# Kernel tuning notes

Measured on AMD Instinct MI355X. Metric: run time of the kernel, lower is better.

Reference implementation:

```python
import jax, jax.numpy as jnp
import numpy as np

N, F, B, H = 4096, 64, 16, 8  # nodes, feat dim, graphs, GAT heads


def _graph():
    # symmetric random graph (avg deg ~8), plus exact 2-hop and 3-hop edge lists
    # (this reproduces torch_sparse.spspmm with coalesced=True on the boolean structure)
    rng = np.random.default_rng(0)
    s = rng.integers(0, N, 8192)
    d = rng.integers(0, N, 8192)
    m = s != d
    s, d = s[m], d[m]
    rows = np.concatenate([s, d]).astype(np.int64)
    cols = np.concatenate([d, s]).astype(np.int64)
    key = np.unique(rows * N + cols)
    rows, cols = key // N, key % N
    A = np.zeros((N, N), np.float32)
    A[rows, cols] = 1.0
    A2 = (A @ A) > 0
    A3 = (A2.astype(np.float32) @ A) > 0
    np.fill_diagonal(A2, False)  # GATConv/GCNConv remove then re-add self-loops
    np.fill_diagonal(A3, False)
    e1 = np.stack([rows, cols]).astype(np.int64)
    e2 = np.stack(np.nonzero(A2)).astype(np.int64)
    e3 = np.stack(np.nonzero(A3)).astype(np.int64)
    return e1, e2, e3


def _sl(ei, n):
    loops = jnp.arange(n, dtype=ei.dtype)
    return jnp.concatenate([ei, jnp.stack([loops, loops])], axis=1)


def _seg_softmax(logits, seg, n):
    m = jax.ops.segment_max(logits, seg, num_segments=n)
    e = jnp.exp(logits - m[seg])
    s = jax.ops.segment_sum(e, seg, num_segments=n)
    return e / s[seg]


def _gat(x, ei, W, a_src, a_dst, b, heads):
    # PyG GATConv: per-head linear, edge attention logits, softmax over incoming edges
    n = x.shape[0]
    d = a_src.shape[1]
    h = (x @ W).reshape(n, heads, d)  # [N,H,D]
    src, dst = ei[0], ei[1]
    al = jnp.einsum('nhd,hd->nh', h, a_src)
    ar = jnp.einsum('nhd,hd->nh', h, a_dst)
    logit = jax.nn.leaky_relu(al[src] + ar[dst], 0.2)  # [E,H]
    alpha = _seg_softmax(logit, dst, n)
    out = jax.ops.segment_sum(alpha[:, :, None] * h[src], dst, num_segments=n)
    return out.reshape(n, heads * d) + b


def _gcn(x, ei, W, b):
    n = x.shape[0]
    src, dst = ei[0], ei[1]
    h = x @ W
    deg = jax.ops.segment_sum(jnp.ones(src.shape, x.dtype), dst, num_segments=n)
    dinv = jnp.where(deg > 0, deg ** -0.5, 0.0)
    norm = dinv[src] * dinv[dst]
    return jax.ops.segment_sum(norm[:, None] * h[src], dst, num_segments=n) + b


def setup_inputs():
    key = jax.random.key(0)
    ks = iter(jax.random.split(key, 40))
    e1, e2, e3 = _graph()
    p = lambda *shape: jax.random.normal(next(ks), shape, jnp.float32) * 0.1
    return dict(
        x=jax.random.normal(next(ks), (N, F), jnp.float32),
        edge_index=jnp.asarray(e1), edge_index2=jnp.asarray(e2), edge_index3=jnp.asarray(e3),
        batch=jnp.asarray(np.repeat(np.arange(B), N // B)),
        g1_W=p(F, H * F), g1_as=p(H, F), g1_ad=p(H, F), g1_b=p(H * F),
        g2_W=p(H * F, F), g2_as=p(1, F), g2_ad=p(1, F), g2_b=p(F),
        gfc_W=p(F, F), gfc_b=p(F), gfc1_W=p(F, 128), gfc1_b=p(128),
        gout_W=p(128, F), gout_b=p(F),
        c2_W=p(F, 2 * F), c2_b=p(2 * F), c3_W=p(2 * F, 4 * F), c3_b=p(4 * F),
        A_W=p(4 * F, F), A_b=p(F), B_W=p(2 * F, F), B_b=p(F),
        Wih=p(F, 3 * F), Whh=p(F, 3 * F), bih=p(3 * F), bhh=p(3 * F),
        f1_W=p(F, 128), f1_b=p(128), f2_W=p(128, 120), f2_b=p(120),
    )


def reference(x, edge_index, edge_index2, edge_index3, batch,
              g1_W, g1_as, g1_ad, g1_b, g2_W, g2_as, g2_ad, g2_b,
              gfc_W, gfc_b, gfc1_W, gfc1_b, gout_W, gout_b,
              c2_W, c2_b, c3_W, c3_b, A_W, A_b, B_W, B_b,
              Wih, Whh, bih, bhh, f1_W, f1_b, f2_W, f2_b):
    n = x.shape[0]
    e1, e2, e3 = _sl(edge_index, n), _sl(edge_index2, n), _sl(edge_index3, n)

    def gat_block(xin, ei):  # inner GAT module (eval mode: dropouts are identity)
        h = jax.nn.elu(_gat(xin, ei, g1_W, g1_as, g1_ad, g1_b, H))
        h = jax.nn.relu(_gat(h, ei, g2_W, g2_as, g2_ad, g2_b, 1))
        h = jax.nn.relu(h @ gfc_W + gfc_b)
        h = jax.nn.relu(h @ gfc1_W + gfc1_b)
        return h @ gout_W + gout_b

    h1 = jax.nn.relu(gat_block(x, e1))
    h2 = jax.nn.relu(_gcn(h1, e1, c2_W, c2_b))
    h3 = jax.nn.relu(_gcn(h2, e1, c3_W, c3_b))            # [N,4F]
    h4 = jax.nn.relu(gat_block(x, e2))
    h5 = jax.nn.relu(_gcn(h4, e2, c2_W, c2_b))            # [N,2F]
    h6 = jax.nn.relu(gat_block(x, e3))                     # [N,F]

    # GateUpdate
    b_ = h5 @ B_W + B_b
    a_ = h3 @ A_W + A_b
    z = jax.nn.sigmoid(a_ + b_)
    hg = z * b_ + (1 - z) * a_
    # GRUCell(h6, hg)
    gi = h6 @ Wih + bih
    gh = hg @ Whh + bhh
    r = jax.nn.sigmoid(gi[:, :F] + gh[:, :F])
    zz = jax.nn.sigmoid(gi[:, F:2 * F] + gh[:, F:2 * F])
    nn_ = jnp.tanh(gi[:, 2 * F:] + r * gh[:, 2 * F:])
    cc = (1 - zz) * nn_ + zz * hg

    g = jax.ops.segment_max(cc, batch, num_segments=B)    # global_max_pool -> [B,F]
    g = jax.nn.relu(g @ f1_W + f1_b)
    return g @ f2_W + f2_b                                 # [B,120]
```

## Files before the change

### kernel.cpp

```cpp
#include <hip/hip_runtime.h>
#include <math.h>

#define NN 4096
#define NG 16
#define WB() __builtin_amdgcn_wave_barrier()

__global__ void rowptr3_kernel(const int* __restrict__ ea, int Ea,
                               const int* __restrict__ eb, int Eb,
                               const int* __restrict__ ec, int Ec,
                               int* __restrict__ rpa, int* __restrict__ rpb, int* __restrict__ rpc){
    int t = blockIdx.x * blockDim.x + threadIdx.x;
    int set = t / (NN + 1), i = t % (NN + 1);
    if (set >= 3) return;
    const int* e0 = set == 0 ? ea : set == 1 ? eb : ec;
    int E        = set == 0 ? Ea : set == 1 ? Eb : Ec;
    int* rp      = set == 0 ? rpa : set == 1 ? rpb : rpc;
    if (i == NN){ rp[NN] = E; return; }
    int lo = 0, hi = E;
    while (lo < hi){ int mid = (lo + hi) >> 1; if (e0[mid] < i) lo = mid + 1; else hi = mid; }
    rp[i] = lo;
}

__global__ void dinv2_kernel(const int* __restrict__ rp1, const int* __restrict__ rp2,
                             float* __restrict__ dinv1, float* __restrict__ dinv2){
    int t = blockIdx.x * blockDim.x + threadIdx.x;
    int set = t >> 12, i = t & (NN - 1);
    if (set >= 2) return;
    const int* rp = set ? rp2 : rp1;
    float deg = (float)(rp[i+1] - rp[i] + 1);
    (set ? dinv2 : dinv1)[i] = 1.0f / sqrtf(deg);
}

__global__ __launch_bounds__(256)
void gemm_kernel(const float* __restrict__ A, const float* __restrict__ W,
                 const float* __restrict__ bias, float* __restrict__ C,
                 int K, int Nc, int act){
    __shared__ float As[64][17];
    __shared__ float Bs[16][64];
    const int tid = threadIdx.x;
    const int tx = tid & 15, ty = tid >> 4;
    const int row0 = blockIdx.y * 64, col0 = blockIdx.x * 64;
    float acc[4][4] = {};
    for (int k0 = 0; k0 < K; k0 += 16){
        {   int idx = tid * 4; int r = idx >> 4, kk = idx & 15;
            float4 av = *reinterpret_cast<const float4*>(&A[(size_t)(row0 + r) * K + k0 + kk]);
            As[r][kk+0]=av.x; As[r][kk+1]=av.y; As[r][kk+2]=av.z; As[r][kk+3]=av.w; }
        {   int idx = tid * 4; int r = idx >> 6, cc = idx & 63;
            float4 wv = *reinterpret_cast<const float4*>(&W[(size_t)(k0 + r) * Nc + col0 + cc]);
            *reinterpret_cast<float4*>(&Bs[r][cc]) = wv; }
        __syncthreads();
        #pragma unroll
        for (int kk = 0; kk < 16; ++kk){
            float a[4], b[4];
            #pragma unroll
            for (int i = 0; i < 4; ++i) a[i] = As[ty*4+i][kk];
            #pragma unroll
            for (int j = 0; j < 4; ++j) b[j] = Bs[kk][tx*4+j];
            #pragma unroll
            for (int i = 0; i < 4; ++i)
                #pragma unroll
                for (int j = 0; j < 4; ++j) acc[i][j] += a[i]*b[j];
        }
        __syncthreads();
    }
    #pragma unroll
    for (int i = 0; i < 4; ++i){
        int r = row0 + ty*4 + i;
        #pragma unroll
        for (int j = 0; j < 4; ++j){
            int c = col0 + tx*4 + j;
            float v = acc[i][j] + (bias ? bias[c] : 0.0f);
            if (act == 1) v = fmaxf(v, 0.0f);
            C[(size_t)r * Nc + c] = v;
        }
    }
}

__global__ __launch_bounds__(256)
void gemm32_kernel(const float* __restrict__ A, const float* __restrict__ W,
                   const float* __restrict__ bias, float* __restrict__ C,
                   int K, int Nc, int act){
    __shared__ float As[32][17];
    __shared__ float Bs[16][64];
    const int tid = threadIdx.x;
    const int tx = tid & 15, ty = tid >> 4;
    const int row0 = blockIdx.y * 32, col0 = blockIdx.x * 64;
    float acc[2][4] = {};
    for (int k0 = 0; k0 < K; k0 += 16){
        {   int idx = tid * 2; int r = idx >> 4, kk = idx & 15;
            float2 av = *reinterpret_cast<const float2*>(&A[(size_t)(row0 + r) * K + k0 + kk]);
            As[r][kk] = av.x; As[r][kk+1] = av.y; }
        {   int idx = tid * 4; int r = idx >> 6, cc = idx & 63;
            *reinterpret_cast<float4*>(&Bs[r][cc]) =
                *reinterpret_cast<const float4*>(&W[(size_t)(k0 + r) * Nc + col0 + cc]); }
        __syncthreads();
        #pragma unroll
        for (int kk = 0; kk < 16; ++kk){
            float a0 = As[ty*2][kk], a1 = As[ty*2+1][kk];
            float b[4];
            #pragma unroll
            for (int j = 0; j < 4; ++j) b[j] = Bs[kk][tx*4+j];
            #pragma unroll
            for (int j = 0; j < 4; ++j){ acc[0][j] += a0*b[j]; acc[1][j] += a1*b[j]; }
        }
        __syncthreads();
    }
    #pragma unroll
    for (int i = 0; i < 2; ++i){
        int r = row0 + ty*2 + i;
        #pragma unroll
        for (int j = 0; j < 4; ++j){
            int c = col0 + tx*4 + j;
            float v = acc[i][j] + (bias ? bias[c] : 0.0f);
            if (act == 1) v = fmaxf(v, 0.0f);
            C[(size_t)r * Nc + c] = v;
        }
    }
}

__global__ __launch_bounds__(256)
void attn_dot8_kernel(const float* __restrict__ h,
                      const float* __restrict__ a_src, const float* __restrict__ a_dst,
                      float* __restrict__ al, float* __restrict__ ar){
    const int lane = threadIdx.x & 63, wid = threadIdx.x >> 6;
    const int n = blockIdx.x * 4 + wid;
    float x[8], y[8];
    #pragma unroll
    for (int c = 0; c < 8; ++c){
        float v = h[(size_t)n*512 + c*64 + lane];
        x[c] = v * a_src[c*64 + lane];
        y[c] = v * a_dst[c*64 + lane];
    }
    #pragma unroll
    for (int off = 1; off < 64; off <<= 1){
        #pragma unroll
        for (int c = 0; c < 8; ++c){
            x[c] += __shfl_xor(x[c], off);
            y[c] += __shfl_xor(y[c], off);
        }
    }
    if (lane == 0){
        #pragma unroll
        for (int c = 0; c < 8; ++c){ al[n*8 + c] = x[c]; ar[n*8 + c] = y[c]; }
    }
}

__global__ __launch_bounds__(256)
void attn_dot1_kernel(const float* __restrict__ h,
                      const float* __restrict__ a_src, const float* __restrict__ a_dst,
                      float* __restrict__ al, float* __restrict__ ar){
    const int lane = threadIdx.x & 63, wid = threadIdx.x >> 6;
    const int n = blockIdx.x * 4 + wid;
    float v = h[(size_t)n*64 + lane];
    float x = v * a_src[lane], y = v * a_dst[lane];
    #pragma unroll
    for (int off = 1; off < 64; off <<= 1){ x += __shfl_xor(x, off); y += __shfl_xor(y, off); }
    if (lane == 0){ al[n] = x; ar[n] = y; }
}

__global__ __launch_bounds__(64)
void gat_agg8_wave_kernel(const float* __restrict__ hfeat,
                          const float* __restrict__ al, const float* __restrict__ ar,
                          const int* __restrict__ rpA, const int* __restrict__ rpB, const int* __restrict__ rpC,
                          const int* __restrict__ clA, const int* __restrict__ clB, const int* __restrict__ clC,
                          const float* __restrict__ bias, float* __restrict__ out){
    const int bid = blockIdx.x;
    const int set = bid >> 12, i = bid & (NN - 1);
    const int lane = threadIdx.x;
    const int* rowptr = set == 0 ? rpA : set == 1 ? rpB : rpC;
    const int* cols   = set == 0 ? clA : set == 1 ? clB : clC;
    const int start = rowptr[i], end = rowptr[i+1];
    const int deg = end - start;

    float al_i[8], ar_i[8];
    {
        float4 t0 = *reinterpret_cast<const float4*>(&al[(size_t)i*8]);
        float4 t1 = *reinterpret_cast<const float4*>(&al[(size_t)i*8+4]);
        al_i[0]=t0.x; al_i[1]=t0.y; al_i[2]=t0.z; al_i[3]=t0.w;
        al_i[4]=t1.x; al_i[5]=t1.y; al_i[6]=t1.z; al_i[7]=t1.w;
        float4 u0 = *reinterpret_cast<const float4*>(&ar[(size_t)i*8]);
        float4 u1 = *reinterpret_cast<const float4*>(&ar[(size_t)i*8+4]);
        ar_i[0]=u0.x; ar_i[1]=u0.y; ar_i[2]=u0.z; ar_i[3]=u0.w;
        ar_i[4]=u1.x; ar_i[5]=u1.y; ar_i[6]=u1.z; ar_i[7]=u1.w;
    }

    float m[8], s[8];
    #pragma unroll
    for (int h = 0; h < 8; ++h){ m[h] = -1e30f; s[h] = 0.f; }
    for (int k = start + lane; k < end; k += 64){
        int j = cols[k];
        float4 t0 = *reinterpret_cast<const float4*>(&al[(size_t)j*8]);
        float4 t1 = *reinterpret_cast<const float4*>(&al[(size_t)j*8+4]);
        float av[8] = {t0.x,t0.y,t0.z,t0.w,t1.x,t1.y,t1.z,t1.w};
        #pragma unroll
        for (int h = 0; h < 8; ++h){
            float x = av[h] + ar_i[h];
            x = x >= 0.f ? x : 0.2f * x;
            float mn = fmaxf(m[h], x);
            s[h] = s[h] * __expf(m[h] - mn) + __expf(x - mn);
            m[h] = mn;
        }
    }
    if (lane == 0){
        #pragma unroll
        for (int h = 0; h < 8; ++h){
            float x = al_i[h] + ar_i[h];
            x = x >= 0.f ? x : 0.2f * x;
            float mn = fmaxf(m[h], x);
            s[h] = s[h] * __expf(m[h] - mn) + __expf(x - mn);
            m[h] = mn;
        }
    }
    #pragma unroll
    for (int off = 1; off < 64; off <<= 1){
        #pragma unroll
        for (int h = 0; h < 8; ++h){
            float m2 = __shfl_xor(m[h], off), s2 = __shfl_xor(s[h], off);
            float mn = fmaxf(m[h], m2);
            s[h] = s[h] * __expf(m[h] - mn) + s2 * __expf(m2 - mn);
            m[h] = mn;
        }
    }

    __shared__ int   sbuf[64];
    __shared__ float wbuf[64][9];
    const int c0 = 4*lane, c1 = 256 + 4*lane;
    const int h0 = lane >> 4, h1 = 4 + h0;
    float4 A0 = {0.f,0.f,0.f,0.f}, A1 = {0.f,0.f,0.f,0.f};
    for (int k0 = 0; k0 < deg; k0 += 64){
        int cnt = min(64, deg - k0);
        if (lane < cnt) sbuf[lane] = cols[start + k0 + lane];
        __syncthreads();
        if (lane < cnt){
            int j = sbuf[lane];
            float4 t0 = *reinterpret_cast<const float4*>(&al[(size_t)j*8]);
            float4 t1 = *reinterpret_cast<const float4*>(&al[(size_t)j*8+4]);
            float av[8] = {t0.x,t0.y,t0.z,t0.w,t1.x,t1.y,t1.z,t1.w};
            #pragma unroll
            for (int h = 0; h < 8; ++h){
                float x = av[h] + ar_i[h];
                x = x >= 0.f ? x : 0.2f * x;
                wbuf[lane][h] = __expf(x - m[h]);
            }
        }
        __syncthreads();
        int e = 0;
        for (; e + 4 <= cnt; e += 4){
            int j0 = sbuf[e], j1 = sbuf[e+1], j2 = sbuf[e+2], j3 = sbuf[e+3];
            const float* q0 = &hfeat[(size_t)j0*512];
            const float* q1 = &hfeat[(size_t)j1*512];
            const float* q2 = &hfeat[(size_t)j2*512];
            const float* q3 = &hfeat[(size_t)j3*512];
            float4 v00 = *reinterpret_cast<const float4*>(q0 + c0);
            float4 v01 = *reinterpret_cast<const float4*>(q0 + c1);
            float4 v10 = *reinterpret_cast<const float4*>(q1 + c0);
            float4 v11 = *reinterpret_cast<const float4*>(q1 + c1);
            float4 v20 = *reinterpret_cast<const float4*>(q2 + c0);
            float4 v21 = *reinterpret_cast<const float4*>(q2 + c1);
            float4 v30 = *reinterpret_cast<const float4*>(q3 + c0);
            float4 v31 = *reinterpret_cast<const float4*>(q3 + c1);
            float w00 = wbuf[e  ][h0], w01 = wbuf[e  ][h1];
            float w10 = wbuf[e+1][h0], w11 = wbuf[e+1][h1];
            float w20 = wbuf[e+2][h0], w21 = wbuf[e+2][h1];
            float w30 = wbuf[e+3][h0], w31 = wbuf[e+3][h1];
            A0.x += w00*v00.x; A0.y += w00*v00.y; A0.z += w00*v00.z; A0.w += w00*v00.w;
            A1.x += w01*v01.x; A1.y += w01*v01.y; A1.z += w01*v01.z; A1.w += w01*v01.w;
            A0.x += w10*v10.x; A0.y += w10*v10.y; A0.z += w10*v10.z; A0.w += w10*v10.w;
            A1.x += w11*v11.x; A1.y += w11*v11.y; A1.z += w11*v11.z; A1.w += w11*v11.w;
            A0.x += w20*v20.x; A0.y += w20*v20.y; A0.z += w20*v20.z; A0.w += w20*v20.w;
            A1.x += w21*v21.x; A1.y += w21*v21.y; A1.z += w21*v21.z; A1.w += w21*v21.w;
            A0.x += w30*v30.x; A0.y += w30*v30.y; A0.z += w30*v30.z; A0.w += w30*v30.w;
            A1.x += w31*v31.x; A1.y += w31*v31.y; A1.z += w31*v31.z; A1.w += w31*v31.w;
        }
        for (; e < cnt; ++e){
            int j = sbuf[e];
            const float* hp = &hfeat[(size_t)j*512];
            float w0 = wbuf[e][h0], w1 = wbuf[e][h1];
            float4 v0 = *reinterpret_cast<const float4*>(hp + c0);
            float4 v1 = *reinterpret_cast<const float4*>(hp + c1);
            A0.x += w0*v0.x; A0.y += w0*v0.y; A0.z += w0*v0.z; A0.w += w0*v0.w;
            A1.x += w1*v1.x; A1.y += w1*v1.y; A1.z += w1*v1.z; A1.w += w1*v1.w;
        }
        __syncthreads();
    }
    {
        float x0 = al_i[h0] + ar_i[h0]; x0 = x0 >= 0.f ? x0 : 0.2f*x0;
        float x1 = al_i[h1] + ar_i[h1]; x1 = x1 >= 0.f ? x1 : 0.2f*x1;
        float w0 = __expf(x0 - m[h0]), w1 = __expf(x1 - m[h1]);
        float4 hv0 = *reinterpret_cast<const float4*>(&hfeat[(size_t)i*512 + c0]);
        float4 hv1 = *reinterpret_cast<const float4*>(&hfeat[(size_t)i*512 + c1]);
        A0.x += w0*hv0.x; A0.y += w0*hv0.y; A0.z += w0*hv0.z; A0.w += w0*hv0.w;
        A1.x += w1*hv1.x; A1.y += w1*hv1.y; A1.z += w1*hv1.z; A1.w += w1*hv1.w;
        float inv0 = 1.f / s[h0], inv1 = 1.f / s[h1];
        float4 b0 = *reinterpret_cast<const float4*>(&bias[c0]);
        float4 b1 = *reinterpret_cast<const float4*>(&bias[c1]);
        float4 o0, o1;
        o0.x = A0.x*inv0 + b0.x; o0.y = A0.y*inv0 + b0.y;
        o0.z = A0.z*inv0 + b0.z; o0.w = A0.w*inv0 + b0.w;
        o1.x = A1.x*inv1 + b1.x; o1.y = A1.y*inv1 + b1.y;
        o1.z = A1.z*inv1 + b1.z; o1.w = A1.w*inv1 + b1.w;
        o0.x = o0.x > 0.f ? o0.x : __expf(o0.x) - 1.f;
        o0.y = o0.y > 0.f ? o0.y : __expf(o0.y) - 1.f;
        o0.z = o0.z > 0.f ? o0.z : __expf(o0.z) - 1.f;
        o0.w = o0.w > 0.f ? o0.w : __expf(o0.w) - 1.f;
        o1.x = o1.x > 0.f ? o1.x : __expf(o1.x) - 1.f;
        o1.y = o1.y > 0.f ? o1.y : __expf(o1.y) - 1.f;
        o1.z = o1.z > 0.f ? o1.z : __expf(o1.z) - 1.f;
        o1.w = o1.w > 0.f ? o1.w : __expf(o1.w) - 1.f;
        *reinterpret_cast<float4*>(&out[(size_t)bid*512 + c0]) = o0;
        *reinterpret_cast<float4*>(&out[(size_t)bid*512 + c1]) = o1;
    }
}

template<int BLOCK, int NHEADS>
__global__ __launch_bounds__(BLOCK)
void gat_agg_kernel(const float* __restrict__ hfeat,
                    const float* __restrict__ al, const float* __restrict__ ar,
                    const int* __restrict__ rpA, const int* __restrict__ rpB, const int* __restrict__ rpC,
                    const int* __restrict__ clA, const int* __restrict__ clB, const int* __restrict__ clC,
                    const float* __restrict__ bias, float* __restrict__ out,
                    int act, int sharedfeat){
    constexpr int TD    = NHEADS * 64;
    constexpr int CHUNK = BLOCK / NHEADS;
    const int bid = blockIdx.x;
    const int set = bid >> 12, i = bid & (NN - 1);
    const int tid = threadIdx.x;
    const int* rowptr = set == 0 ? rpA : set == 1 ? rpB : rpC;
    const int* cols   = set == 0 ? clA : set == 1 ? clB : clC;
    const int base = sharedfeat ? 0 : set * NN;
    const int start = rowptr[i], end = rowptr[i+1];

    float al_i[NHEADS], ar_i[NHEADS];
    #pragma unroll
    for (int h = 0; h < NHEADS; ++h){
        al_i[h] = al[(size_t)(base + i)*NHEADS + h];
        ar_i[h] = ar[(size_t)(base + i)*NHEADS + h];
    }
    float m[NHEADS], s[NHEADS];
    #pragma unroll
    for (int h = 0; h < NHEADS; ++h){ m[h] = -1e30f; s[h] = 0.f; }
    for (int k = start + tid; k < end; k += BLOCK){
        int j = cols[k];
        #pragma unroll
        for (int h = 0; h < NHEADS; ++h){
            float x = al[(size_t)(base + j)*NHEADS + h] + ar_i[h];
            x = x >= 0.f ? x : 0.2f * x;
            float mn = fmaxf(m[h], x);
            s[h] = s[h] * __expf(m[h] - mn) + __expf(x - mn);
            m[h] = mn;
        }
    }
    if (tid == 0){
        #pragma unroll
        for (int h = 0; h < NHEADS; ++h){
            float x = al_i[h] + ar_i[h];
            x = x >= 0.f ? x : 0.2f * x;
            float mn = fmaxf(m[h], x);
            s[h] = s[h] * __expf(m[h] - mn) + __expf(x - mn);
            m[h] = mn;
        }
    }
    #pragma unroll
    for (int off = 1; off < 64; off <<= 1){
        #pragma unroll
        for (int h = 0; h < NHEADS; ++h){
            float m2 = __shfl_xor(m[h], off), s2 = __shfl_xor(s[h], off);
            float mn = fmaxf(m[h], m2);
            s[h] = s[h] * __expf(m[h] - mn) + s2 * __expf(m2 - mn);
            m[h] = mn;
        }
    }

    __shared__ int   sbuf[CHUNK];
    __shared__ float wbuf[CHUNK][NHEADS];
    const int deg = end - start;
    float p0 = 0.f, p1 = 0.f, p2 = 0.f, p3 = 0.f;
    for (int k0 = 0; k0 < deg; k0 += CHUNK){
        int cnt = min(CHUNK, deg - k0);
        if (tid < cnt) sbuf[tid] = cols[start + k0 + tid];
        __syncthreads();
        if (tid < cnt){
            float x = al[(size_t)(base + sbuf[tid])*NHEADS] + ar_i[0];
            x = x >= 0.f ? x : 0.2f * x;
            wbuf[tid][0] = __expf(x - m[0]);
        }
        __syncthreads();
        int e = 0;
        for (; e + 8 <= cnt; e += 8){
            int j0 = sbuf[e],   j1 = sbuf[e+1], j2 = sbuf[e+2], j3 = sbuf[e+3];
            int j4 = sbuf[e+4], j5 = sbuf[e+5], j6 = sbuf[e+6], j7 = sbuf[e+7];
            float v0 = hfeat[(size_t)(base + j0)*TD + tid];
            float v1 = hfeat[(size_t)(base + j1)*TD + tid];
            float v2 = hfeat[(size_t)(base + j2)*TD + tid];
            float v3 = hfeat[(size_t)(base + j3)*TD + tid];
            float v4 = hfeat[(size_t)(base + j4)*TD + tid];
            float v5 = hfeat[(size_t)(base + j5)*TD + tid];
            float v6 = hfeat[(size_t)(base + j6)*TD + tid];
            float v7 = hfeat[(size_t)(base + j7)*TD + tid];
            p0 += wbuf[e  ][0] * v0; p1 += wbuf[e+1][0] * v1;
            p2 += wbuf[e+2][0] * v2; p3 += wbuf[e+3][0] * v3;
            p0 += wbuf[e+4][0] * v4; p1 += wbuf[e+5][0] * v5;
            p2 += wbuf[e+6][0] * v6; p3 += wbuf[e+7][0] * v7;
        }
        for (; e < cnt; ++e)
            p0 += wbuf[e][0] * hfeat[(size_t)(base + sbuf[e])*TD + tid];
        __syncthreads();
    }
    float acc = (p0 + p1) + (p2 + p3);
    float x = al_i[0] + ar_i[0];
    x = x >= 0.f ? x : 0.2f * x;
    acc += __expf(x - m[0]) * hfeat[(size_t)(base + i)*TD + tid];
    float v = acc / s[0] + bias[tid];
    if (act == 1) v = fmaxf(v, 0.f);
    else          v = v > 0.f ? v : __expf(v) - 1.f;
    out[(size_t)bid*TD + tid] = v;
}

template<int DIM>
__global__ __launch_bounds__(DIM)
void gcn_agg_kernel(const float* __restrict__ h,
                    const int* __restrict__ rpA, const int* __restrict__ rpB,
                    const int* __restrict__ clA, const int* __restrict__ clB,
                    const float* __restrict__ dvA, const float* __restrict__ dvB,
                    const float* __restrict__ bias, float* __restrict__ out){
    const int bid = blockIdx.x;
    const int set = bid >> 12, i = bid & (NN - 1);
    const int* rowptr = set ? rpB : rpA;
    const int* cols   = set ? clB : clA;
    const float* dinv = set ? dvB : dvA;
    const int c = threadIdx.x;
    const int start = rowptr[i], end = rowptr[i+1];
    const float di = dinv[i];
    const size_t rbase = (size_t)(set * NN) * DIM;
    float self = di * di * h[(size_t)bid * DIM + c];
    float p0 = 0.f, p1 = 0.f, p2 = 0.f, p3 = 0.f;
    int k = start;
    for (; k + 8 <= end; k += 8){
        int j0 = cols[k],   j1 = cols[k+1], j2 = cols[k+2], j3 = cols[k+3];
        int j4 = cols[k+4], j5 = cols[k+5], j6 = cols[k+6], j7 = cols[k+7];
        float v0 = h[rbase + (size_t)j0 * DIM + c];
        float v1 = h[rbase + (size_t)j1 * DIM + c];
        float v2 = h[rbase + (size_t)j2 * DIM + c];
        float v3 = h[rbase + (size_t)j3 * DIM + c];
        float v4 = h[rbase + (size_t)j4 * DIM + c];
        float v5 = h[rbase + (size_t)j5 * DIM + c];
        float v6 = h[rbase + (size_t)j6 * DIM + c];
        float v7 = h[rbase + (size_t)j7 * DIM + c];
        p0 += dinv[j0] * v0; p1 += dinv[j1] * v1;
        p2 += dinv[j2] * v2; p3 += dinv[j3] * v3;
        p0 += dinv[j4] * v4; p1 += dinv[j5] * v5;
        p2 += dinv[j6] * v6; p3 += dinv[j7] * v7;
    }
    for (; k < end; ++k){
        int j = cols[k];
        p0 += dinv[j] * h[rbase + (size_t)j * DIM + c];
    }
    float acc = self + di * ((p0 + p1) + (p2 + p3));
    out[(size_t)bid * DIM + c] = fmaxf(acc + bias[c], 0.f);
}

__global__ __launch_bounds__(256)
void gate_gru_kernel(const float* __restrict__ h3, const float* __restrict__ h5,
                     const float* __restrict__ h6,
                     const float* __restrict__ A_W, const float* __restrict__ A_b,
                     const float* __restrict__ B_W, const float* __restrict__ B_b,
                     const float* __restrict__ Wih, const float* __restrict__ bih,
                     const float* __restrict__ Whh, const float* __restrict__ bhh,
                     float* __restrict__ cc){
    __shared__ float l3[4][256];
    __shared__ float l5[4][128];
    __shared__ float l6[4][64];
    __shared__ float lhg[4][64];
    const int lane = threadIdx.x & 63, wid = threadIdx.x >> 6;
    const int r = blockIdx.x * 4 + wid;
    for (int c = lane; c < 256; c += 64) l3[wid][c] = h3[(size_t)r*256 + c];
    for (int c = lane; c < 128; c += 64) l5[wid][c] = h5[(size_t)r*128 + c];
    l6[wid][lane] = h6[(size_t)r*64 + lane];
    WB();
    float a = A_b[lane];
    #pragma unroll 8
    for (int k = 0; k < 256; ++k) a += l3[wid][k] * A_W[k*64 + lane];
    float b = B_b[lane];
    #pragma unroll 8
    for (int k = 0; k < 128; ++k) b += l5[wid][k] * B_W[k*64 + lane];
    float z = 1.f / (1.f + expf(-(a + b)));
    float hg = z * b + (1.f - z) * a;
    lhg[wid][lane] = hg;
    WB();
    float gi0 = bih[lane], gi1 = bih[64 + lane], gi2 = bih[128 + lane];
    float gh0 = bhh[lane], gh1 = bhh[64 + lane], gh2 = bhh[128 + lane];
    #pragma unroll 4
    for (int k = 0; k < 64; ++k){
        float v6 = l6[wid][k], vh = lhg[wid][k];
        gi0 += v6 * Wih[k*192 + lane];
        gi1 += v6 * Wih[k*192 + 64 + lane];
        gi2 += v6 * Wih[k*192 + 128 + lane];
        gh0 += vh * Whh[k*192 + lane];
        gh1 += vh * Whh[k*192 + 64 + lane];
        gh2 += vh * Whh[k*192 + 128 + lane];
    }
    float rr = 1.f / (1.f + expf(-(gi0 + gh0)));
    float zz = 1.f / (1.f + expf(-(gi1 + gh1)));
    float nn = tanhf(gi2 + rr * gh2);
    cc[(size_t)r*64 + lane] = (1.f - zz) * nn + zz * hg;
}

__global__ __launch_bounds__(256)
void head_kernel(const float* __restrict__ cc,
                 const float* __restrict__ f1_W, const float* __restrict__ f1_b,
                 const float* __restrict__ f2_W, const float* __restrict__ f2_b,
                 float* __restrict__ out){
    const int b = blockIdx.x, tid = threadIdx.x;
    const int c = tid & 63, grp = tid >> 6;
    __shared__ float red4[4][64];
    __shared__ float gmax[64];
    __shared__ float fgs[128];
    const float* base = cc + (size_t)(b * (NN / NG)) * 64;
    float m = -1e30f;
    #pragma unroll 8
    for (int n = grp; n < NN / NG; n += 4) m = fmaxf(m, base[n * 64 + c]);
    red4[grp][c] = m;
    __syncthreads();
    if (tid < 64)
        gmax[tid] = fmaxf(fmaxf(red4[0][tid], red4[1][tid]),
                          fmaxf(red4[2][tid], red4[3][tid]));
    __syncthreads();
    if (tid < 128){
        float acc = 0.f;
        #pragma unroll
        for (int k = 0; k < 64; ++k) acc += gmax[k] * f1_W[k * 128 + tid];
        fgs[tid] = fmaxf(acc + f1_b[tid], 0.f);
    }
    __syncthreads();
    if (tid < 120){
        float acc = 0.f;
        #pragma unroll
        for (int k = 0; k < 128; ++k) acc += fgs[k] * f2_W[k * 120 + tid];
        out[b * 120 + tid] = acc + f2_b[tid];
    }
}

extern "C" void kernel_launch(void* const* d_in, const int* in_sizes, int n_in,
                              void* d_out, int out_size, void* d_ws, size_t ws_size,
                              hipStream_t stream){
    const float* x  = (const float*)d_in[0];
    const int* e1 = (const int*)d_in[1]; const int E1 = in_sizes[1] / 2;
    const int* e2 = (const int*)d_in[2]; const int E2 = in_sizes[2] / 2;
    const int* e3 = (const int*)d_in[3]; const int E3 = in_sizes[3] / 2;
    const float* g1_W  = (const float*)d_in[5];
    const float* g1_as = (const float*)d_in[6];
    const float* g1_ad = (const float*)d_in[7];
    const float* g1_b  = (const float*)d_in[8];
    const float* g2_W  = (const float*)d_in[9];
    const float* g2_as = (const float*)d_in[10];
    const float* g2_ad = (const float*)d_in[11];
    const float* g2_b  = (const float*)d_in[12];
    const float* gfc_W = (const float*)d_in[13];
    const float* gfc_b = (const float*)d_in[14];
    const float* gfc1_W= (const float*)d_in[15];
    const float* gfc1_b= (const float*)d_in[16];
    const float* gout_W= (const float*)d_in[17];
    const float* gout_b= (const float*)d_in[18];
    const float* c2_W  = (const float*)d_in[19];
    const float* c2_b  = (const float*)d_in[20];
    const float* c3_W  = (const float*)d_in[21];
    const float* c3_b  = (const float*)d_in[22];
    const float* A_W   = (const float*)d_in[23];
    const float* A_b   = (const float*)d_in[24];
    const float* B_W   = (const float*)d_in[25];
    const float* B_b   = (const float*)d_in[26];
    const float* Wih   = (const float*)d_in[27];
    const float* Whh   = (const float*)d_in[28];
    const float* bih   = (const float*)d_in[29];
    const float* bhh   = (const float*)d_in[30];
    const float* f1_W  = (const float*)d_in[31];
    const float* f1_b  = (const float*)d_in[32];
    const float* f2_W  = (const float*)d_in[33];
    const float* f2_b  = (const float*)d_in[34];
    float* out = (float*)d_out;

    int* ip = (int*)d_ws;
    int* rp1 = ip; int* rp2 = ip + 4100; int* rp3 = ip + 8200;
    float* fb = (float*)(ip + 12300);
    size_t o = 0;
    auto alloc = [&](size_t nf){ float* p = fb + o; o += nf; return p; };
    float* dinv1 = alloc(NN);
    float* dinv2 = alloc(NN);
    float* hbuf  = alloc((size_t)NN*512);
    float* al1   = alloc((size_t)NN*8);
    float* ar1   = alloc((size_t)NN*8);
    float* bigA  = alloc((size_t)3*NN*512);
    float* t2    = alloc((size_t)3*NN*64);
    float* al2   = alloc((size_t)3*NN);
    float* ar2   = alloc((size_t)3*NN);
    (void)ws_size; (void)n_in; (void)out_size;

    float* eluo3 = bigA;
    float* g2o   = bigA;
    float* fc1   = bigA + (size_t)786432;
    float* fc2   = bigA + (size_t)1572864;
    float* houts = hbuf;
    float* h1    = houts;
    float* h6    = houts + (size_t)2*NN*64;
    float* gcnx2 = bigA + (size_t)3145728;
    float* h25   = bigA + (size_t)4194304;
    float* h2    = h25;
    float* h5    = h25 + (size_t)NN*128;
    float* gcnx3 = bigA;
    float* h3    = bigA + (size_t)1048576;
    float* ccb   = bigA + (size_t)4456448;
    const int* cols1 = e1 + E1; const int* cols2 = e2 + E2; const int* cols3 = e3 + E3;

    rowptr3_kernel<<<(3*(NN+1)+255)/256, 256, 0, stream>>>(e1, E1, e2, E2, e3, E3, rp1, rp2, rp3);
    dinv2_kernel<<<2*NN/256, 256, 0, stream>>>(rp1, rp2, dinv1, dinv2);

    gemm_kernel<<<dim3(8, 64), 256, 0, stream>>>(x, g1_W, nullptr, hbuf, 64, 512, 0);
    attn_dot8_kernel<<<NN/4, 256, 0, stream>>>(hbuf, g1_as, g1_ad, al1, ar1);
    gat_agg8_wave_kernel<<<3*NN, 64, 0, stream>>>(hbuf, al1, ar1,
        rp1, rp2, rp3, cols1, cols2, cols3, g1_b, eluo3);
    gemm32_kernel<<<dim3(1, 384), 256, 0, stream>>>(eluo3, g2_W, nullptr, t2, 512, 64, 0);
    attn_dot1_kernel<<<3*NN/4, 256, 0, stream>>>(t2, g2_as, g2_ad, al2, ar2);
    gat_agg_kernel<64,1><<<3*NN, 64, 0, stream>>>(t2, al2, ar2,
        rp1, rp2, rp3, cols1, cols2, cols3, g2_b, g2o, 1, 0);
    gemm32_kernel<<<dim3(1, 384), 256, 0, stream>>>(g2o, gfc_W, gfc_b, fc1, 64, 64, 1);
    gemm_kernel<<<dim3(2, 192), 256, 0, stream>>>(fc1, gfc1_W, gfc1_b, fc2, 64, 128, 1);
    gemm32_kernel<<<dim3(1, 384), 256, 0, stream>>>(fc2, gout_W, gout_b, houts, 128, 64, 1);

    gemm_kernel<<<dim3(2, 128), 256, 0, stream>>>(houts, c2_W, nullptr, gcnx2, 64, 128, 0);
    gcn_agg_kernel<128><<<2*NN, 128, 0, stream>>>(gcnx2, rp1, rp2, cols1, cols2,
                                                  dinv1, dinv2, c2_b, h25);
    gemm_kernel<<<dim3(4, 64), 256, 0, stream>>>(h2, c3_W, nullptr, gcnx3, 128, 256, 0);
    gcn_agg_kernel<256><<<NN, 256, 0, stream>>>(gcnx3, rp1, rp1, cols1, cols1,
                                                dinv1, dinv1, c3_b, h3);

    gate_gru_kernel<<<NN/4, 256, 0, stream>>>(h3, h5, h6, A_W, A_b, B_W, B_b,
                                              Wih, bih, Whh, bhh, ccb);

    head_kernel<<<NG, 256, 0, stream>>>(ccb, f1_W, f1_b, f2_W, f2_b, out);
}
```

Measured before the change: 376.6 us.

## Split 8-head GAT aggregation into softmax-stats pass and half-head aggregation pass

The fused 8-head GAT aggregation kernel is split in two. A first kernel computes the per-node, per-head softmax max and sum and writes them to new workspace buffers. A second kernel, launched with twice as many blocks, has each block handle 4 heads (256 columns) of one node. This is meant to expose more parallelism and lower per-block latency on high-degree 2-hop and 3-hop neighbourhoods. In exchange it adds a kernel launch, an extra global round trip for the stats, and redundant reads of column indices and attention logits across the two halves.

New measurement: 371.0 us. No clear change (-1.5%).

```diff
diff --git a/kernel.cpp b/kernel.cpp
--- a/kernel.cpp
+++ b/kernel.cpp
@@ -159,18 +159,16 @@
 }
 
 __global__ __launch_bounds__(64)
-void gat_agg8_wave_kernel(const float* __restrict__ hfeat,
-                          const float* __restrict__ al, const float* __restrict__ ar,
-                          const int* __restrict__ rpA, const int* __restrict__ rpB, const int* __restrict__ rpC,
-                          const int* __restrict__ clA, const int* __restrict__ clB, const int* __restrict__ clC,
-                          const float* __restrict__ bias, float* __restrict__ out){
-    const int bid = blockIdx.x;
-    const int set = bid >> 12, i = bid & (NN - 1);
+void attn_ms8_kernel(const float* __restrict__ al, const float* __restrict__ ar,
+                     const int* __restrict__ rpA, const int* __restrict__ rpB, const int* __restrict__ rpC,
+                     const int* __restrict__ clA, const int* __restrict__ clB, const int* __restrict__ clC,
+                     float* __restrict__ m8, float* __restrict__ s8){
+    const int g = blockIdx.x;
+    const int set = g >> 12, i = g & (NN - 1);
     const int lane = threadIdx.x;
     const int* rowptr = set == 0 ? rpA : set == 1 ? rpB : rpC;
     const int* cols   = set == 0 ? clA : set == 1 ? clB : clC;
     const int start = rowptr[i], end = rowptr[i+1];
-    const int deg = end - start;
 
     float al_i[8], ar_i[8];
     {
@@ -183,7 +181,6 @@
         ar_i[0]=u0.x; ar_i[1]=u0.y; ar_i[2]=u0.z; ar_i[3]=u0.w;
         ar_i[4]=u1.x; ar_i[5]=u1.y; ar_i[6]=u1.z; ar_i[7]=u1.w;
     }
-
     float m[8], s[8];
     #pragma unroll
     for (int h = 0; h < 8; ++h){ m[h] = -1e30f; s[h] = 0.f; }
@@ -221,95 +218,94 @@
             m[h] = mn;
         }
     }
+    if (lane == 0){
+        #pragma unroll
+        for (int h = 0; h < 8; ++h){ m8[(size_t)g*8 + h] = m[h]; s8[(size_t)g*8 + h] = s[h]; }
+    }
+}
+
+__global__ __launch_bounds__(64)
+void gat_agg8_p2_kernel(const float* __restrict__ hfeat,
+                        const float* __restrict__ al, const float* __restrict__ ar,
+                        const float* __restrict__ m8, const float* __restrict__ s8,
+                        const int* __restrict__ rpA, const int* __restrict__ rpB, const int* __restrict__ rpC,
+                        const int* __restrict__ clA, const int* __restrict__ clB, const int* __restrict__ clC,
+                        const float* __restrict__ bias, float* __restrict__ out){
+    const int bid = blockIdx.x;
+    const int g = bid >> 1, half = bid & 1;
+    const int set = g >> 12, i = g & (NN - 1);
+    const int lane = threadIdx.x;
+    const int* rowptr = set == 0 ? rpA : set == 1 ? rpB : rpC;
+    const int* cols   = set == 0 ? clA : set == 1 ? clB : clC;
+    const int start = rowptr[i], end = rowptr[i+1];
+    const int deg = end - start;
+    const int hb = half * 4;
+    const int c0 = half * 256 + 4 * lane;
+    const int hr = lane >> 4;
+
+    float4 mv = *reinterpret_cast<const float4*>(&m8[(size_t)g*8 + hb]);
+    float4 sv = *reinterpret_cast<const float4*>(&s8[(size_t)g*8 + hb]);
+    float mh[4] = {mv.x, mv.y, mv.z, mv.w};
+    float sh[4] = {sv.x, sv.y, sv.z, sv.w};
+    float4 arv = *reinterpret_cast<const float4*>(&ar[(size_t)i*8 + hb]);
+    float ar_i[4] = {arv.x, arv.y, arv.z, arv.w};
+    float4 alv = *reinterpret_cast<const float4*>(&al[(size_t)i*8 + hb]);
+    float al_i[4] = {alv.x, alv.y, alv.z, alv.w};
 
     __shared__ int   sbuf[64];
-    __shared__ float wbuf[64][9];
-    const int c0 = 4*lane, c1 = 256 + 4*lane;
-    const int h0 = lane >> 4, h1 = 4 + h0;
-    float4 A0 = {0.f,0.f,0.f,0.f}, A1 = {0.f,0.f,0.f,0.f};
+    __shared__ float wbuf[64][5];
+    float4 A0 = {0.f, 0.f, 0.f, 0.f};
     for (int k0 = 0; k0 < deg; k0 += 64){
         int cnt = min(64, deg - k0);
-        if (lane < cnt) sbuf[lane] = cols[start + k0 + lane];
-        __syncthreads();
         if (lane < cnt){
-            int j = sbuf[lane];
-            float4 t0 = *reinterpret_cast<const float4*>(&al[(size_t)j*8]);
-            float4 t1 = *reinterpret_cast<const float4*>(&al[(size_t)j*8+4]);
-            float av[8] = {t0.x,t0.y,t0.z,t0.w,t1.x,t1.y,t1.z,t1.w};
+            int j = cols[start + k0 + lane];
+            sbuf[lane] = j;
+            float4 av = *reinterpret_cast<const float4*>(&al[(size_t)j*8 + hb]);
+            float a4[4] = {av.x, av.y, av.z, av.w};
             #pragma unroll
-            for (int h = 0; h < 8; ++h){
-                float x = av[h] + ar_i[h];
+            for (int h = 0; h < 4; ++h){
+                float x = a4[h] + ar_i[h];
                 x = x >= 0.f ? x : 0.2f * x;
-                wbuf[lane][h] = __expf(x - m[h]);
+                wbuf[lane][h] = __expf(x - mh[h]);
             }
         }
         __syncthreads();
         int e = 0;
         for (; e + 4 <= cnt; e += 4){
             int j0 = sbuf[e], j1 = sbuf[e+1], j2 = sbuf[e+2], j3 = sbuf[e+3];
-            const float* q0 = &hfeat[(size_t)j0*512];
-            const float* q1 = &hfeat[(size_t)j1*512];
-            const float* q2 = &hfeat[(size_t)j2*512];
-            const float* q3 = &hfeat[(size_t)j3*512];
-            float4 v00 = *reinterpret_cast<const float4*>(q0 + c0);
-            float4 v01 = *reinterpret_cast<const float4*>(q0 + c1);
-            float4 v10 = *reinterpret_cast<const float4*>(q1 + c0);
-            float4 v11 = *reinterpret_cast<const float4*>(q1 + c1);
-            float4 v20 = *reinterpret_cast<const float4*>(q2 + c0);
-            float4 v21 = *reinterpret_cast<const float4*>(q2 + c1);
-            float4 v30 = *reinterpret_cast<const float4*>(q3 + c0);
-            float4 v31 = *reinterpret_cast<const float4*>(q3 + c1);
-            float w00 = wbuf[e  ][h0], w01 = wbuf[e  ][h1];
-            float w10 = wbuf[e+1][h0], w11 = wbuf[e+1][h1];
-            float w20 = wbuf[e+2][h0], w21 = wbuf[e+2][h1];
-            float w30 = wbuf[e+3][h0], w31 = wbuf[e+3][h1];
-            A0.x += w00*v00.x; A0.y += w00*v00.y; A0.z += w00*v00.z; A0.w += w00*v00.w;
-            A1.x += w01*v01.x; A1.y += w01*v01.y; A1.z += w01*v01.z; A1.w += w01*v01.w;
-            A0.x += w10*v10.x; A0.y += w10*v10.y; A0.z += w10*v10.z; A0.w += w10*v10.w;
-            A1.x += w11*v11.x; A1.y += w11*v11.y; A1.z += w11*v11.z; A1.w += w11*v11.w;
-            A0.x += w20*v20.x; A0.y += w20*v20.y; A0.z += w20*v20.z; A0.w += w20*v20.w;
-            A1.x += w21*v21.x; A1.y += w21*v21.y; A1.z += w21*v21.z; A1.w += w21*v21.w;
-            A0.x += w30*v30.x; A0.y += w30*v30.y; A0.z += w30*v30.z; A0.w += w30*v30.w;
-            A1.x += w31*v31.x; A1.y += w31*v31.y; A1.z += w31*v31.z; A1.w += w31*v31.w;
+            float4 v0 = *reinterpret_cast<const float4*>(&hfeat[(size_t)j0*512 + c0]);
+            float4 v1 = *reinterpret_cast<const float4*>(&hfeat[(size_t)j1*512 + c0]);
+            float4 v2 = *reinterpret_cast<const float4*>(&hfeat[(size_t)j2*512 + c0]);
+            float4 v3 = *reinterpret_cast<const float4*>(&hfeat[(size_t)j3*512 + c0]);
+            float w0 = wbuf[e][hr], w1 = wbuf[e+1][hr], w2 = wbuf[e+2][hr], w3 = wbuf[e+3][hr];
+            A0.x += w0*v0.x; A0.y += w0*v0.y; A0.z += w0*v0.z; A0.w += w0*v0.w;
+            A0.x += w1*v1.x; A0.y += w1*v1.y; A0.z += w1*v1.z; A0.w += w1*v1.w;
+            A0.x += w2*v2.x; A0.y += w2*v2.y; A0.z += w2*v2.z; A0.w += w2*v2.w;
+            A0.x += w3*v3.x; A0.y += w3*v3.y; A0.z += w3*v3.z; A0.w += w3*v3.w;
         }
         for (; e < cnt; ++e){
             int j = sbuf[e];
-            const float* hp = &hfeat[(size_t)j*512];
-            float w0 = wbuf[e][h0], w1 = wbuf[e][h1];
-            float4 v0 = *reinterpret_cast<const float4*>(hp + c0);
-            float4 v1 = *reinterpret_cast<const float4*>(hp + c1);
-            A0.x += w0*v0.x; A0.y += w0*v0.y; A0.z += w0*v0.z; A0.w += w0*v0.w;
-            A1.x += w1*v1.x; A1.y += w1*v1.y; A1.z += w1*v1.z; A1.w += w1*v1.w;
-        }
-        __syncthreads();
-    }
-    {
-        float x0 = al_i[h0] + ar_i[h0]; x0 = x0 >= 0.f ? x0 : 0.2f*x0;
-        float x1 = al_i[h1] + ar_i[h1]; x1 = x1 >= 0.f ? x1 : 0.2f*x1;
-        float w0 = __expf(x0 - m[h0]), w1 = __expf(x1 - m[h1]);
-        float4 hv0 = *reinterpret_cast<const float4*>(&hfeat[(size_t)i*512 + c0]);
-        float4 hv1 = *reinterpret_cast<const float4*>(&hfeat[(size_t)i*512 + c1]);
-        A0.x += w0*hv0.x; A0.y += w0*hv0.y; A0.z += w0*hv0.z; A0.w += w0*hv0.w;
-        A1.x += w1*hv1.x; A1.y += w1*hv1.y; A1.z += w1*hv1.z; A1.w += w1*hv1.w;
-        float inv0 = 1.f / s[h0], inv1 = 1.f / s[h1];
-        float4 b0 = *reinterpret_cast<const float4*>(&bias[c0]);
-        float4 b1 = *reinterpret_cast<const float4*>(&bias[c1]);
-        float4 o0, o1;
-        o0.x = A0.x*inv0 + b0.x; o0.y = A0.y*inv0 + b0.y;
-        o0.z = A0.z*inv0 + b0.z; o0.w = A0.w*inv0 + b0.w;
-        o1.x = A1.x*inv1 + b1.x; o1.y = A1.y*inv1 + b1.y;
-        o1.z = A1.z*inv1 + b1.z; o1.w = A1.w*inv1 + b1.w;
-        o0.x = o0.x > 0.f ? o0.x : __expf(o0.x) - 1.f;
-        o0.y = o0.y > 0.f ? o0.y : __expf(o0.y) - 1.f;
-        o0.z = o0.z > 0.f ? o0.z : __expf(o0.z) - 1.f;
-        o0.w = o0.w > 0.f ? o0.w : __expf(o0.w) - 1.f;
-        o1.x = o1.x > 0.f ? o1.x : __expf(o1.x) - 1.f;
-        o1.y = o1.y > 0.f ? o1.y : __expf(o1.y) - 1.f;
-        o1.z = o1.z > 0.f ? o1.z : __expf(o1.z) - 1.f;
-        o1.w = o1.w > 0.f ? o1.w : __expf(o1.w) - 1.f;
-        *reinterpret_cast<float4*>(&out[(size_t)bid*512 + c0]) = o0;
-        *reinterpret_cast<float4*>(&out[(size_t)bid*512 + c1]) = o1;
-    }
+            float4 v = *reinterpret_cast<const float4*>(&hfeat[(size_t)j*512 + c0]);
+            float w = wbuf[e][hr];
+            A0.x += w*v.x; A0.y += w*v.y; A0.z += w*v.z; A0.w += w*v.w;
+        }
+        __syncthreads();
+    }
+    float x = al_i[hr] + ar_i[hr];
+    x = x >= 0.f ? x : 0.2f * x;
+    float ws = __expf(x - mh[hr]);
+    float4 hv = *reinterpret_cast<const float4*>(&hfeat[(size_t)i*512 + c0]);
+    A0.x += ws*hv.x; A0.y += ws*hv.y; A0.z += ws*hv.z; A0.w += ws*hv.w;
+    float inv = 1.f / sh[hr];
+    float4 bv = *reinterpret_cast<const float4*>(&bias[c0]);
+    float4 o;
+    o.x = A0.x*inv + bv.x; o.y = A0.y*inv + bv.y;
+    o.z = A0.z*inv + bv.z; o.w = A0.w*inv + bv.w;
+    o.x = o.x > 0.f ? o.x : __expf(o.x) - 1.f;
+    o.y = o.y > 0.f ? o.y : __expf(o.y) - 1.f;
+    o.z = o.z > 0.f ? o.z : __expf(o.z) - 1.f;
+    o.w = o.w > 0.f ? o.w : __expf(o.w) - 1.f;
+    *reinterpret_cast<float4*>(&out[(size_t)g*512 + c0]) = o;
 }
 
 template<int BLOCK, int NHEADS>
@@ -593,6 +589,8 @@
     float* t2    = alloc((size_t)3*NN*64);
     float* al2   = alloc((size_t)3*NN);
     float* ar2   = alloc((size_t)3*NN);
+    float* m8buf = alloc((size_t)3*NN*8);
+    float* s8buf = alloc((size_t)3*NN*8);
     (void)ws_size; (void)n_in; (void)out_size;
 
     float* eluo3 = bigA;
@@ -616,7 +614,9 @@
 
     gemm_kernel<<<dim3(8, 64), 256, 0, stream>>>(x, g1_W, nullptr, hbuf, 64, 512, 0);
     attn_dot8_kernel<<<NN/4, 256, 0, stream>>>(hbuf, g1_as, g1_ad, al1, ar1);
-    gat_agg8_wave_kernel<<<3*NN, 64, 0, stream>>>(hbuf, al1, ar1,
+    attn_ms8_kernel<<<3*NN, 64, 0, stream>>>(al1, ar1,
+        rp1, rp2, rp3, cols1, cols2, cols3, m8buf, s8buf);
+    gat_agg8_p2_kernel<<<6*NN, 64, 0, stream>>>(hbuf, al1, ar1, m8buf, s8buf,
         rp1, rp2, rp3, cols1, cols2, cols3, g1_b, eluo3);
     gemm32_kernel<<<dim3(1, 384), 256, 0, stream>>>(eluo3, g2_W, nullptr, t2, 512, 64, 0);
     attn_dot1_kernel<<<3*NN/4, 256, 0, stream>>>(t2, g2_as, g2_ad, al2, ar2);
```
